# Kernel optimization log

Measured on AMD Instinct MI355X. Metric: run time of the kernel, lower is better.

The kernel has to match this reference:

```python
import jax, jax.numpy as jnp
import numpy as np

N_NODES = 100000
N_EDGES = 1600000
D_IN = 128
D_HID = 128
N_CLASSES = 10


def setup_inputs() -> dict:
    key = jax.random.key(0)
    ks = jax.random.split(key, 9)
    x = jax.random.normal(ks[0], (N_NODES, D_IN), dtype=jnp.float32)
    edge_index = jax.random.randint(ks[1], (2, N_EDGES), 0, N_NODES, dtype=jnp.int64)
    edge_attr = jax.random.uniform(ks[2], (N_EDGES,), dtype=jnp.float32)
    s1 = 1.0 / np.sqrt(D_IN)
    s2 = 1.0 / np.sqrt(D_HID)
    W1 = jax.random.uniform(ks[3], (D_IN, D_HID), jnp.float32, -s1, s1)
    b1 = jnp.zeros((D_HID,), jnp.float32)
    W2 = jax.random.uniform(ks[4], (D_HID, D_HID), jnp.float32, -s2, s2)
    b2 = jnp.zeros((D_HID,), jnp.float32)
    Wm = jax.random.uniform(ks[5], (D_HID, N_CLASSES), jnp.float32, -s2, s2)
    bm = jax.random.uniform(ks[6], (N_CLASSES,), jnp.float32, -s2, s2)
    return {"x": x, "edge_index": edge_index, "edge_attr": edge_attr,
            "W1": W1, "b1": b1, "W2": W2, "b2": b2, "Wm": Wm, "bm": bm}


def _gcn_norm(edge_index, edge_attr, n_nodes):
    # PyG GCNConv default: add self-loops (weight 1), symmetric normalization.
    src, dst = edge_index[0], edge_index[1]
    loop = jnp.arange(n_nodes, dtype=src.dtype)
    src_f = jnp.concatenate([src, loop])
    dst_f = jnp.concatenate([dst, loop])
    w = jnp.concatenate([edge_attr, jnp.ones((n_nodes,), edge_attr.dtype)])
    deg = jax.ops.segment_sum(w, dst_f, num_segments=n_nodes)  # in-degree
    dinv = jnp.where(deg > 0, jax.lax.rsqrt(deg), 0.0)
    norm = dinv[src_f] * w * dinv[dst_f]  # [E + N]
    return src_f, dst_f, norm


def _gcn_conv(x, src_f, dst_f, norm, W, b, n_nodes):
    h = x @ W                                   # [N, D] dense transform first
    msg = h[src_f] * norm[:, None]              # gather + scale  [E+N, D]
    agg = jax.ops.segment_sum(msg, dst_f, num_segments=n_nodes)  # scatter-add
    return agg + b


def reference(x, edge_index, edge_attr, W1, b1, W2, b2, Wm, bm):
    n = x.shape[0]
    src_f, dst_f, norm = _gcn_norm(edge_index, edge_attr, n)
    h = jax.nn.relu(_gcn_conv(x, src_f, dst_f, norm, W1, b1, n))
    h = jax.nn.relu(_gcn_conv(h, src_f, dst_f, norm, W2, b2, n))
    # F.dropout(training=False) is identity in eval mode
    pooled = jnp.mean(h, axis=0)                # global mean pool -> [D_HID]
    return pooled @ Wm + bm                     # [N_CLASSES]
```

## Files before the change

### kernel.cpp

```cpp
#include <hip/hip_runtime.h>

#define N_NODES_C 100000
#define N_EDGES_C 1600000
#define D_C 128
#define N_CLASSES_C 10
#define POOL_BLOCKS_C 1024
#define NBUCKET 391
#define BUCKET_CAP 4608
#define BPAD 16
#define EPB 4096
#define NB_A ((N_EDGES_C + EPB - 1) / EPB)

using bf16x8 = __attribute__((ext_vector_type(8))) short;
using f32x4  = __attribute__((ext_vector_type(4))) float;

__device__ __forceinline__ unsigned int pack_bf2(float a, float b) {
    unsigned int ua = __float_as_uint(a);
    unsigned int ub = __float_as_uint(b);
    ua = (ua + 0x7FFFu + ((ua >> 16) & 1u)) >> 16;
    ub = (ub + 0x7FFFu + ((ub >> 16) & 1u)) & 0xFFFF0000u;
    return ua | ub;
}

__device__ __forceinline__ void bf8_fma(uint4 r, float v, float* acc) {
    acc[0] = fmaf(v, __uint_as_float(r.x << 16), acc[0]);
    acc[1] = fmaf(v, __uint_as_float(r.x & 0xFFFF0000u), acc[1]);
    acc[2] = fmaf(v, __uint_as_float(r.y << 16), acc[2]);
    acc[3] = fmaf(v, __uint_as_float(r.y & 0xFFFF0000u), acc[3]);
    acc[4] = fmaf(v, __uint_as_float(r.z << 16), acc[4]);
    acc[5] = fmaf(v, __uint_as_float(r.z & 0xFFFF0000u), acc[5]);
    acc[6] = fmaf(v, __uint_as_float(r.w << 16), acc[6]);
    acc[7] = fmaf(v, __uint_as_float(r.w & 0xFFFF0000u), acc[7]);
}

__device__ __forceinline__ int edge_word(const int* __restrict__ ei, long long idx, int is64) {
    return is64 ? ei[2 * idx] : ei[idx];
}

__global__ void detect_init_kernel(const int* __restrict__ ei, int* __restrict__ flag,
                                   int* __restrict__ bcnt) {
    int t = threadIdx.x;
    if (blockIdx.x == 0) {
        if (t < 64) {
            int nz = 0;
            for (int i = t; i < 512; i += 64) nz |= ei[2 * i + 1];
            unsigned long long b = __ballot(nz != 0);
            if (t == 0) *flag = (b == 0ULL) ? 1 : 0;
        }
    } else {
        int i = (blockIdx.x - 1) * 256 + t;
        if (i < NBUCKET * BPAD) bcnt[i] = 0;
    }
}

__global__ __launch_bounds__(512) void bucket_fill_kernel(
        const int* __restrict__ ei, const float* __restrict__ attr,
        const int* __restrict__ flag, int* __restrict__ bcnt, int2* __restrict__ bkt) {
    __shared__ int2 stage[EPB];
    __shared__ unsigned short sbin[EPB];
    __shared__ int hist[512];
    __shared__ int lstart[512];
    __shared__ int cursor[NBUCKET];
    __shared__ int gbase[NBUCKET];

    const int t = threadIdx.x;
    const long long e0 = (long long)blockIdx.x * EPB;
    const int n = (N_EDGES_C - e0 < EPB) ? (int)(N_EDGES_C - e0) : EPB;
    const int is64 = *flag;

    hist[t] = 0;
    __syncthreads();

    int  myb[8];
    int2 myrec[8];
#pragma unroll
    for (int j = 0; j < 8; ++j) {
        int i = t + j * 512;
        myb[j] = -1;
        if (i < n) {
            long long e = e0 + i;
            int s = edge_word(ei, e, is64);
            int d = edge_word(ei, (long long)N_EDGES_C + e, is64);
            float a = attr[e];
            int b = d >> 8;
            myb[j] = b;
            myrec[j].x = s | ((d & 0xFF) << 17);
            myrec[j].y = __float_as_int(a);
            atomicAdd(&hist[b], 1);
        }
    }
    __syncthreads();

    const int myh = hist[t];
    lstart[t] = myh;
    __syncthreads();
    for (int off = 1; off < 512; off <<= 1) {
        int v = lstart[t];
        int add = (t >= off) ? lstart[t - off] : 0;
        __syncthreads();
        lstart[t] = v + add;
        __syncthreads();
    }
    int excl = lstart[t] - myh;
    if (t < NBUCKET) cursor[t] = excl;
    lstart[t] = excl;
    __syncthreads();

#pragma unroll
    for (int j = 0; j < 8; ++j) {
        if (myb[j] >= 0) {
            int slot = atomicAdd(&cursor[myb[j]], 1);
            stage[slot] = myrec[j];
            sbin[slot] = (unsigned short)myb[j];
        }
    }
    if (t < NBUCKET) {
        int k = myh;
        gbase[t] = k ? atomicAdd(&bcnt[t * BPAD], k) : 0;
    }
    __syncthreads();

    for (int i = t; i < n; i += 512) {
        int b = sbin[i];
        int local = gbase[b] + (i - lstart[b]);
        if (local < BUCKET_CAP)
            bkt[(long long)b * BUCKET_CAP + local] = stage[i];
    }
}

__global__ __launch_bounds__(256) void bucket_sort_kernel(
        const int* __restrict__ bcnt, int2* __restrict__ bkt,
        int2* __restrict__ rowinfo, float* __restrict__ dinv) {
    __shared__ int2 recA[BUCKET_CAP];
    __shared__ int2 recB[BUCKET_CAP];
    __shared__ int hist[256], lstart[256], cursor[256];
    __shared__ float degs[256];

    const int b = blockIdx.x, t = threadIdx.x;
    int n = bcnt[b * BPAD];
    if (n > BUCKET_CAP) n = BUCKET_CAP;
    int2* win = bkt + (long long)b * BUCKET_CAP;

    hist[t] = 0;
    degs[t] = 0.f;
    __syncthreads();

    for (int i = t; i < n; i += 256) {
        int2 cv = win[i];
        recA[i] = cv;
        int d = (cv.x >> 17) & 0xFF;
        atomicAdd(&hist[d], 1);
        atomicAdd(&degs[d], __int_as_float(cv.y));
    }
    __syncthreads();

    const int myh = hist[t];
    lstart[t] = myh;
    __syncthreads();
    for (int off = 1; off < 256; off <<= 1) {
        int v = lstart[t];
        int add = (t >= off) ? lstart[t - off] : 0;
        __syncthreads();
        lstart[t] = v + add;
        __syncthreads();
    }
    int excl = lstart[t] - myh;
    cursor[t] = excl;
    lstart[t] = excl;
    __syncthreads();

    for (int i = t; i < n; i += 256) {
        int2 cv = recA[i];
        int d = (cv.x >> 17) & 0xFF;
        int slot = atomicAdd(&cursor[d], 1);
        int2 o;
        o.x = cv.x & 0x1FFFF;
        o.y = cv.y;
        recB[slot] = o;
    }
    __syncthreads();

    for (int i = t; i < n; i += 256) win[i] = recB[i];

    int node = b * 256 + t;
    if (node < N_NODES_C) {
        int2 ri;
        ri.x = b * BUCKET_CAP + lstart[t];
        ri.y = myh;
        rowinfo[node] = ri;
        dinv[node] = rsqrtf(1.0f + degs[t]);
    }
}

__global__ __launch_bounds__(256) void convert_x_kernel(const float* __restrict__ x,
                                                        unsigned short* __restrict__ xb) {
    long long i = (long long)blockIdx.x * blockDim.x + threadIdx.x;
    const long long n8 = (long long)N_NODES_C * D_C / 8;
    if (i >= n8) return;
    const float4* p = (const float4*)x + i * 2;
    float4 a = p[0], b = p[1];
    uint4 o;
    o.x = pack_bf2(a.x, a.y);
    o.y = pack_bf2(a.z, a.w);
    o.z = pack_bf2(b.x, b.y);
    o.w = pack_bf2(b.z, b.w);
    ((uint4*)xb)[i] = o;
}

__global__ __launch_bounds__(256) void prep_w_kernel(const float* __restrict__ W1,
                                                     const float* __restrict__ W2,
                                                     unsigned short* __restrict__ Wp1,
                                                     unsigned short* __restrict__ Wp2) {
    const float* W = (blockIdx.x & 8) ? W2 : W1;
    unsigned short* Wp = (blockIdx.x & 8) ? Wp2 : Wp1;
    const int n = blockIdx.x & 7;
    const int t = threadIdx.x;
    const int s = t >> 6, l = t & 63;
    const int col = n * 16 + (l & 15);
    const int k0 = s * 32 + (l >> 4) * 8;
    float v[8];
#pragma unroll
    for (int j = 0; j < 8; ++j) v[j] = W[(k0 + j) * 128 + col];
    uint4 o;
    o.x = pack_bf2(v[0], v[1]);
    o.y = pack_bf2(v[2], v[3]);
    o.z = pack_bf2(v[4], v[5]);
    o.w = pack_bf2(v[6], v[7]);
    ((uint4*)Wp)[(n * 4 + s) * 64 + l] = o;
}

__global__ __launch_bounds__(256) void gemm_mfma(const unsigned short* __restrict__ A,
                                                 const unsigned short* __restrict__ Wp,
                                                 const float* __restrict__ dinv,
                                                 unsigned short* __restrict__ H,
                                                 int nrows) {
    __shared__ unsigned short Bl[2048 * 8];
    {
        const uint4* src = (const uint4*)Wp;
        uint4* dst = (uint4*)Bl;
        for (int i = threadIdx.x; i < 2048; i += 256) dst[i] = src[i];
    }
    __syncthreads();

    const int wid = threadIdx.x >> 6, lane = threadIdx.x & 63;
    const int rowA = lane & 15, kg = lane >> 4;
    const int r0 = blockIdx.x * 128 + wid * 32;

    bf16x8 afr[2][4];
#pragma unroll
    for (int m = 0; m < 2; ++m) {
        int row = r0 + m * 16 + rowA;
        if (row >= nrows) row = nrows - 1;
        const unsigned short* xp = A + (long long)row * D_C + kg * 8;
#pragma unroll
        for (int s = 0; s < 4; ++s) afr[m][s] = *(const bf16x8*)(xp + s * 32);
    }

    f32x4 acc[2][8];
#pragma unroll
    for (int m = 0; m < 2; ++m)
#pragma unroll
        for (int n = 0; n < 8; ++n) acc[m][n] = (f32x4){0.f, 0.f, 0.f, 0.f};

#pragma unroll
    for (int n = 0; n < 8; ++n) {
#pragma unroll
        for (int s = 0; s < 4; ++s) {
            bf16x8 bfr = *(const bf16x8*)(Bl + ((n * 4 + s) * 64 + lane) * 8);
            acc[0][n] = __builtin_amdgcn_mfma_f32_16x16x32_bf16(afr[0][s], bfr, acc[0][n], 0, 0, 0);
            acc[1][n] = __builtin_amdgcn_mfma_f32_16x16x32_bf16(afr[1][s], bfr, acc[1][n], 0, 0, 0);
        }
    }

    const int colb = lane & 15, rq = lane >> 4;
#pragma unroll
    for (int m = 0; m < 2; ++m) {
#pragma unroll
        for (int q = 0; q < 4; ++q) {
            int row = r0 + m * 16 + rq * 4 + q;
            if (row >= nrows) continue;
            float sc = dinv[row];
#pragma unroll
            for (int n = 0; n < 8; ++n) {
                unsigned int u = __float_as_uint(acc[m][n][q] * sc);
                u = (u + 0x7FFFu + ((u >> 16) & 1u)) >> 16;
                H[(long long)row * D_C + n * 16 + colb] = (unsigned short)u;
            }
        }
    }
}

template <int MODE>
__global__ __launch_bounds__(256) void agg_kernel(
        const unsigned short* __restrict__ h, const float* __restrict__ dinv,
        const int2* __restrict__ rowinfo, const int2* __restrict__ recs,
        const float* __restrict__ bias, void* __restrict__ out_v) {
    __shared__ float pool[128];
    if (MODE == 1) {
        if (threadIdx.x < 128) pool[threadIdx.x] = 0.f;
        __syncthreads();
    }
    const int g    = threadIdx.x >> 4;
    const int sub  = threadIdx.x & 15;
    const int lane = threadIdx.x & 63;
    const int grp  = lane >> 4;

    const float4 bA = *(const float4*)(bias + sub * 8);
    const float4 bB = *(const float4*)(bias + sub * 8 + 4);
    float p[8] = {0.f, 0.f, 0.f, 0.f, 0.f, 0.f, 0.f, 0.f};

    for (int i = blockIdx.x * 16 + g; i < N_NODES_C; i += gridDim.x * 16) {
        const float di = dinv[i];
        const int2 ri = rowinfo[i];
        const int2* row = recs + ri.x;
        const int m = ri.y;

        float acc[8] = {0.f, 0.f, 0.f, 0.f, 0.f, 0.f, 0.f, 0.f};
        {
            uint4 r = *(const uint4*)(h + (long long)i * D_C + sub * 8);
            bf8_fma(r, 1.0f, acc);
        }
        int j = 0;
        for (; j + 7 < m; j += 8) {
            int2 c0 = row[j + 0], c1 = row[j + 1], c2 = row[j + 2], c3 = row[j + 3];
            int2 c4 = row[j + 4], c5 = row[j + 5], c6 = row[j + 6], c7 = row[j + 7];
            uint4 r0 = *(const uint4*)(h + (long long)c0.x * D_C + sub * 8);
            uint4 r1 = *(const uint4*)(h + (long long)c1.x * D_C + sub * 8);
            uint4 r2 = *(const uint4*)(h + (long long)c2.x * D_C + sub * 8);
            uint4 r3 = *(const uint4*)(h + (long long)c3.x * D_C + sub * 8);
            uint4 r4 = *(const uint4*)(h + (long long)c4.x * D_C + sub * 8);
            uint4 r5 = *(const uint4*)(h + (long long)c5.x * D_C + sub * 8);
            uint4 r6 = *(const uint4*)(h + (long long)c6.x * D_C + sub * 8);
            uint4 r7 = *(const uint4*)(h + (long long)c7.x * D_C + sub * 8);
            bf8_fma(r0, __int_as_float(c0.y), acc);
            bf8_fma(r1, __int_as_float(c1.y), acc);
            bf8_fma(r2, __int_as_float(c2.y), acc);
            bf8_fma(r3, __int_as_float(c3.y), acc);
            bf8_fma(r4, __int_as_float(c4.y), acc);
            bf8_fma(r5, __int_as_float(c5.y), acc);
            bf8_fma(r6, __int_as_float(c6.y), acc);
            bf8_fma(r7, __int_as_float(c7.y), acc);
        }
        for (; j + 3 < m; j += 4) {
            int2 c0 = row[j + 0], c1 = row[j + 1], c2 = row[j + 2], c3 = row[j + 3];
            uint4 r0 = *(const uint4*)(h + (long long)c0.x * D_C + sub * 8);
            uint4 r1 = *(const uint4*)(h + (long long)c1.x * D_C + sub * 8);
            uint4 r2 = *(const uint4*)(h + (long long)c2.x * D_C + sub * 8);
            uint4 r3 = *(const uint4*)(h + (long long)c3.x * D_C + sub * 8);
            bf8_fma(r0, __int_as_float(c0.y), acc);
            bf8_fma(r1, __int_as_float(c1.y), acc);
            bf8_fma(r2, __int_as_float(c2.y), acc);
            bf8_fma(r3, __int_as_float(c3.y), acc);
        }
        for (; j < m; ++j) {
            int2 cv = row[j];
            uint4 r = *(const uint4*)(h + (long long)cv.x * D_C + sub * 8);
            bf8_fma(r, __int_as_float(cv.y), acc);
        }

        float o[8];
        o[0] = fmaxf(fmaf(acc[0], di, bA.x), 0.f);
        o[1] = fmaxf(fmaf(acc[1], di, bA.y), 0.f);
        o[2] = fmaxf(fmaf(acc[2], di, bA.z), 0.f);
        o[3] = fmaxf(fmaf(acc[3], di, bA.w), 0.f);
        o[4] = fmaxf(fmaf(acc[4], di, bB.x), 0.f);
        o[5] = fmaxf(fmaf(acc[5], di, bB.y), 0.f);
        o[6] = fmaxf(fmaf(acc[6], di, bB.z), 0.f);
        o[7] = fmaxf(fmaf(acc[7], di, bB.w), 0.f);

        if (MODE == 0) {
            uint4 pk;
            pk.x = pack_bf2(o[0], o[1]);
            pk.y = pack_bf2(o[2], o[3]);
            pk.z = pack_bf2(o[4], o[5]);
            pk.w = pack_bf2(o[6], o[7]);
            *(uint4*)((unsigned short*)out_v + (long long)i * D_C + sub * 8) = pk;
        } else {
#pragma unroll
            for (int k = 0; k < 8; ++k) p[k] += o[k];
        }
    }

    if (MODE == 1) {
#pragma unroll
        for (int k = 0; k < 8; ++k) {
            p[k] += __shfl_xor(p[k], 16);
            p[k] += __shfl_xor(p[k], 32);
        }
        if (grp == 0) {
#pragma unroll
            for (int k = 0; k < 8; ++k) atomicAdd(&pool[sub * 8 + k], p[k]);
        }
        __syncthreads();
        if (threadIdx.x < 128)
            ((float*)out_v)[blockIdx.x * 128 + threadIdx.x] = pool[threadIdx.x];
    }
}

__global__ __launch_bounds__(1024) void final_kernel(const float* __restrict__ part,
                                                     const float* __restrict__ Wm,
                                                     const float* __restrict__ bm,
                                                     float* __restrict__ out) {
    __shared__ float red[8][128];
    __shared__ float pooled[128];
    int t = threadIdx.x;
    int f = t & 127, c = t >> 7;
    float s = 0.f;
    for (int b = c; b < POOL_BLOCKS_C; b += 8) s += part[b * 128 + f];
    red[c][f] = s;
    __syncthreads();
    if (t < 128) {
        float tot = 0.f;
#pragma unroll
        for (int cc = 0; cc < 8; ++cc) tot += red[cc][t];
        pooled[t] = tot / (float)N_NODES_C;
    }
    __syncthreads();
    if (t < N_CLASSES_C) {
        float o = bm[t];
        for (int ff = 0; ff < 128; ++ff) o = fmaf(pooled[ff], Wm[ff * N_CLASSES_C + t], o);
        out[t] = o;
    }
}

extern "C" void kernel_launch(void* const* d_in, const int* in_sizes, int n_in,
                              void* d_out, int out_size, void* d_ws, size_t ws_size,
                              hipStream_t stream) {
    const float* x    = (const float*)d_in[0];
    const int*   ei   = (const int*)d_in[1];
    const float* attr = (const float*)d_in[2];
    const float* W1   = (const float*)d_in[3];
    const float* b1   = (const float*)d_in[4];
    const float* W2   = (const float*)d_in[5];
    const float* b2   = (const float*)d_in[6];
    const float* Wm   = (const float*)d_in[7];
    const float* bm   = (const float*)d_in[8];
    float* out = (float*)d_out;

    char* ws = (char*)d_ws;
    size_t off = 0;
    auto alloc = [&](size_t bytes) -> char* {
        char* p = ws + off;
        off += (bytes + 255) & ~(size_t)255;
        return p;
    };
    int*            flag    = (int*)alloc(4);
    int*            bcnt    = (int*)alloc((size_t)NBUCKET * BPAD * 4);
    int2*           rowinfo = (int2*)alloc((size_t)N_NODES_C * 8);
    float*          dinv    = (float*)alloc((size_t)N_NODES_C * 4);
    int2*           bkt     = (int2*)alloc((size_t)NBUCKET * BUCKET_CAP * 8);
    float*          part    = (float*)alloc((size_t)POOL_BLOCKS_C * 128 * 4);
    unsigned short* Wp1     = (unsigned short*)alloc(2048 * 8 * 2);
    unsigned short* Wp2     = (unsigned short*)alloc(2048 * 8 * 2);
    unsigned short* xb      = (unsigned short*)alloc((size_t)N_NODES_C * D_C * 2);
    unsigned short* hbuf    = (unsigned short*)alloc((size_t)N_NODES_C * D_C * 2);
    unsigned short* hb2     = (unsigned short*)alloc((size_t)N_NODES_C * D_C * 2);
    (void)ws_size;

    const int ntiles = (N_NODES_C + 127) / 128;
    const int agg_blocks = (N_NODES_C + 15) / 16;
    const int init_blocks = 1 + (NBUCKET * BPAD + 255) / 256;
    const int cvt_blocks = (int)(((long long)N_NODES_C * D_C / 8 + 255) / 256);

    detect_init_kernel<<<init_blocks, 256, 0, stream>>>(ei, flag, bcnt);
    bucket_fill_kernel<<<NB_A, 512, 0, stream>>>(ei, attr, flag, bcnt, bkt);
    bucket_sort_kernel<<<NBUCKET, 256, 0, stream>>>(bcnt, bkt, rowinfo, dinv);
    convert_x_kernel<<<cvt_blocks, 256, 0, stream>>>(x, xb);
    prep_w_kernel<<<16, 256, 0, stream>>>(W1, W2, Wp1, Wp2);

    gemm_mfma<<<ntiles, 256, 0, stream>>>(xb, Wp1, dinv, hbuf, N_NODES_C);
    agg_kernel<0><<<agg_blocks, 256, 0, stream>>>(hbuf, dinv, rowinfo, bkt, b1, hb2);
    gemm_mfma<<<ntiles, 256, 0, stream>>>(hb2, Wp2, dinv, hbuf, N_NODES_C);
    agg_kernel<1><<<POOL_BLOCKS_C, 256, 0, stream>>>(hbuf, dinv, rowinfo, bkt, b2, part);
    final_kernel<<<1, 1024, 0, stream>>>(part, Wm, bm, out);
}
```

Before: 247.9 us.

## Fuse x bf16 conversion into GEMM and process two nodes per group in aggregation

Drops the separate fp32-to-bf16 conversion kernel for x: the first GEMM now reads fp32 rows directly and packs them to bf16 in registers, which removes a full write and re-read of the converted array. The aggregation kernel has each 16-lane group handle two nodes at once, interleaving their edge gathers so more independent loads are in flight. The pooling grid is doubled to match. In exchange, the first GEMM reads twice as many A bytes, and the paired loop raises register pressure while degree imbalance between the two nodes leaves tail work unbalanced.

New measurement: 318.3 us. 28.4% more time.

```diff
diff --git a/kernel.cpp b/kernel.cpp
--- a/kernel.cpp
+++ b/kernel.cpp
@@ -4,7 +4,7 @@
 #define N_EDGES_C 1600000
 #define D_C 128
 #define N_CLASSES_C 10
-#define POOL_BLOCKS_C 1024
+#define POOL_BLOCKS_C 2048
 #define NBUCKET 391
 #define BUCKET_CAP 4608
 #define BPAD 16
@@ -192,21 +192,6 @@
     }
 }
 
-__global__ __launch_bounds__(256) void convert_x_kernel(const float* __restrict__ x,
-                                                        unsigned short* __restrict__ xb) {
-    long long i = (long long)blockIdx.x * blockDim.x + threadIdx.x;
-    const long long n8 = (long long)N_NODES_C * D_C / 8;
-    if (i >= n8) return;
-    const float4* p = (const float4*)x + i * 2;
-    float4 a = p[0], b = p[1];
-    uint4 o;
-    o.x = pack_bf2(a.x, a.y);
-    o.y = pack_bf2(a.z, a.w);
-    o.z = pack_bf2(b.x, b.y);
-    o.w = pack_bf2(b.z, b.w);
-    ((uint4*)xb)[i] = o;
-}
-
 __global__ __launch_bounds__(256) void prep_w_kernel(const float* __restrict__ W1,
                                                      const float* __restrict__ W2,
                                                      unsigned short* __restrict__ Wp1,
@@ -229,7 +214,8 @@
     ((uint4*)Wp)[(n * 4 + s) * 64 + l] = o;
 }
 
-__global__ __launch_bounds__(256) void gemm_mfma(const unsigned short* __restrict__ A,
+template <bool AF32>
+__global__ __launch_bounds__(256) void gemm_mfma(const void* __restrict__ A,
                                                  const unsigned short* __restrict__ Wp,
                                                  const float* __restrict__ dinv,
                                                  unsigned short* __restrict__ H,
@@ -251,9 +237,24 @@
     for (int m = 0; m < 2; ++m) {
         int row = r0 + m * 16 + rowA;
         if (row >= nrows) row = nrows - 1;
-        const unsigned short* xp = A + (long long)row * D_C + kg * 8;
-#pragma unroll
-        for (int s = 0; s < 4; ++s) afr[m][s] = *(const bf16x8*)(xp + s * 32);
+        if constexpr (AF32) {
+            const float* xp = (const float*)A + (long long)row * D_C + kg * 8;
+#pragma unroll
+            for (int s = 0; s < 4; ++s) {
+                float4 lo = *(const float4*)(xp + s * 32);
+                float4 hi = *(const float4*)(xp + s * 32 + 4);
+                uint4 pk;
+                pk.x = pack_bf2(lo.x, lo.y);
+                pk.y = pack_bf2(lo.z, lo.w);
+                pk.z = pack_bf2(hi.x, hi.y);
+                pk.w = pack_bf2(hi.z, hi.w);
+                afr[m][s] = __builtin_bit_cast(bf16x8, pk);
+            }
+        } else {
+            const unsigned short* xp = (const unsigned short*)A + (long long)row * D_C + kg * 8;
+#pragma unroll
+            for (int s = 0; s < 4; ++s) afr[m][s] = *(const bf16x8*)(xp + s * 32);
+        }
     }
 
     f32x4 acc[2][8];
@@ -288,6 +289,59 @@
             }
         }
     }
+}
+
+__device__ __forceinline__ void agg_edges(const unsigned short* __restrict__ h,
+                                          const int2* __restrict__ row,
+                                          int j, int m, int sub, float* acc) {
+    for (; j + 7 < m; j += 8) {
+        int2 c0 = row[j + 0], c1 = row[j + 1], c2 = row[j + 2], c3 = row[j + 3];
+        int2 c4 = row[j + 4], c5 = row[j + 5], c6 = row[j + 6], c7 = row[j + 7];
+        uint4 r0 = *(const uint4*)(h + (long long)c0.x * D_C + sub * 8);
+        uint4 r1 = *(const uint4*)(h + (long long)c1.x * D_C + sub * 8);
+        uint4 r2 = *(const uint4*)(h + (long long)c2.x * D_C + sub * 8);
+        uint4 r3 = *(const uint4*)(h + (long long)c3.x * D_C + sub * 8);
+        uint4 r4 = *(const uint4*)(h + (long long)c4.x * D_C + sub * 8);
+        uint4 r5 = *(const uint4*)(h + (long long)c5.x * D_C + sub * 8);
+        uint4 r6 = *(const uint4*)(h + (long long)c6.x * D_C + sub * 8);
+        uint4 r7 = *(const uint4*)(h + (long long)c7.x * D_C + sub * 8);
+        bf8_fma(r0, __int_as_float(c0.y), acc);
+        bf8_fma(r1, __int_as_float(c1.y), acc);
+        bf8_fma(r2, __int_as_float(c2.y), acc);
+        bf8_fma(r3, __int_as_float(c3.y), acc);
+        bf8_fma(r4, __int_as_float(c4.y), acc);
+        bf8_fma(r5, __int_as_float(c5.y), acc);
+        bf8_fma(r6, __int_as_float(c6.y), acc);
+        bf8_fma(r7, __int_as_float(c7.y), acc);
+    }
+    for (; j + 3 < m; j += 4) {
+        int2 c0 = row[j + 0], c1 = row[j + 1], c2 = row[j + 2], c3 = row[j + 3];
+        uint4 r0 = *(const uint4*)(h + (long long)c0.x * D_C + sub * 8);
+        uint4 r1 = *(const uint4*)(h + (long long)c1.x * D_C + sub * 8);
+        uint4 r2 = *(const uint4*)(h + (long long)c2.x * D_C + sub * 8);
+        uint4 r3 = *(const uint4*)(h + (long long)c3.x * D_C + sub * 8);
+        bf8_fma(r0, __int_as_float(c0.y), acc);
+        bf8_fma(r1, __int_as_float(c1.y), acc);
+        bf8_fma(r2, __int_as_float(c2.y), acc);
+        bf8_fma(r3, __int_as_float(c3.y), acc);
+    }
+    for (; j < m; ++j) {
+        int2 cv = row[j];
+        uint4 r = *(const uint4*)(h + (long long)cv.x * D_C + sub * 8);
+        bf8_fma(r, __int_as_float(cv.y), acc);
+    }
+}
+
+__device__ __forceinline__ void finish_node(const float* acc, float di,
+                                            float4 bA, float4 bB, float* o) {
+    o[0] = fmaxf(fmaf(acc[0], di, bA.x), 0.f);
+    o[1] = fmaxf(fmaf(acc[1], di, bA.y), 0.f);
+    o[2] = fmaxf(fmaf(acc[2], di, bA.z), 0.f);
+    o[3] = fmaxf(fmaf(acc[3], di, bA.w), 0.f);
+    o[4] = fmaxf(fmaf(acc[4], di, bB.x), 0.f);
+    o[5] = fmaxf(fmaf(acc[5], di, bB.y), 0.f);
+    o[6] = fmaxf(fmaf(acc[6], di, bB.z), 0.f);
+    o[7] = fmaxf(fmaf(acc[7], di, bB.w), 0.f);
 }
 
 template <int MODE>
@@ -305,79 +359,103 @@
     const int lane = threadIdx.x & 63;
     const int grp  = lane >> 4;
 
-    const float4 bA = *(const float4*)(bias + sub * 8);
-    const float4 bB = *(const float4*)(bias + sub * 8 + 4);
+    const float4 bA4 = *(const float4*)(bias + sub * 8);
+    const float4 bB4 = *(const float4*)(bias + sub * 8 + 4);
     float p[8] = {0.f, 0.f, 0.f, 0.f, 0.f, 0.f, 0.f, 0.f};
 
-    for (int i = blockIdx.x * 16 + g; i < N_NODES_C; i += gridDim.x * 16) {
-        const float di = dinv[i];
-        const int2 ri = rowinfo[i];
-        const int2* row = recs + ri.x;
-        const int m = ri.y;
-
-        float acc[8] = {0.f, 0.f, 0.f, 0.f, 0.f, 0.f, 0.f, 0.f};
+    for (int i0 = blockIdx.x * 32 + g * 2; i0 < N_NODES_C; i0 += gridDim.x * 32) {
+        const int iA = i0, iB = i0 + 1;
+        const bool hB = (iB < N_NODES_C);
+        const float diA = dinv[iA];
+        const int2 riA = rowinfo[iA];
+        float diB = 0.f;
+        int2 riB = riA;
+        if (hB) { diB = dinv[iB]; riB = rowinfo[iB]; }
+        const int2* rowA = recs + riA.x;
+        const int2* rowB = recs + riB.x;
+        const int mA = riA.y;
+        const int mB = hB ? riB.y : 0;
+
+        float accA[8] = {0.f, 0.f, 0.f, 0.f, 0.f, 0.f, 0.f, 0.f};
+        float accB[8] = {0.f, 0.f, 0.f, 0.f, 0.f, 0.f, 0.f, 0.f};
         {
-            uint4 r = *(const uint4*)(h + (long long)i * D_C + sub * 8);
-            bf8_fma(r, 1.0f, acc);
-        }
+            uint4 sA = *(const uint4*)(h + (long long)iA * D_C + sub * 8);
+            bf8_fma(sA, 1.0f, accA);
+            if (hB) {
+                uint4 sB = *(const uint4*)(h + (long long)iB * D_C + sub * 8);
+                bf8_fma(sB, 1.0f, accB);
+            }
+        }
+
         int j = 0;
-        for (; j + 7 < m; j += 8) {
-            int2 c0 = row[j + 0], c1 = row[j + 1], c2 = row[j + 2], c3 = row[j + 3];
-            int2 c4 = row[j + 4], c5 = row[j + 5], c6 = row[j + 6], c7 = row[j + 7];
-            uint4 r0 = *(const uint4*)(h + (long long)c0.x * D_C + sub * 8);
-            uint4 r1 = *(const uint4*)(h + (long long)c1.x * D_C + sub * 8);
-            uint4 r2 = *(const uint4*)(h + (long long)c2.x * D_C + sub * 8);
-            uint4 r3 = *(const uint4*)(h + (long long)c3.x * D_C + sub * 8);
-            uint4 r4 = *(const uint4*)(h + (long long)c4.x * D_C + sub * 8);
-            uint4 r5 = *(const uint4*)(h + (long long)c5.x * D_C + sub * 8);
-            uint4 r6 = *(const uint4*)(h + (long long)c6.x * D_C + sub * 8);
-            uint4 r7 = *(const uint4*)(h + (long long)c7.x * D_C + sub * 8);
-            bf8_fma(r0, __int_as_float(c0.y), acc);
-            bf8_fma(r1, __int_as_float(c1.y), acc);
-            bf8_fma(r2, __int_as_float(c2.y), acc);
-            bf8_fma(r3, __int_as_float(c3.y), acc);
-            bf8_fma(r4, __int_as_float(c4.y), acc);
-            bf8_fma(r5, __int_as_float(c5.y), acc);
-            bf8_fma(r6, __int_as_float(c6.y), acc);
-            bf8_fma(r7, __int_as_float(c7.y), acc);
-        }
-        for (; j + 3 < m; j += 4) {
-            int2 c0 = row[j + 0], c1 = row[j + 1], c2 = row[j + 2], c3 = row[j + 3];
-            uint4 r0 = *(const uint4*)(h + (long long)c0.x * D_C + sub * 8);
-            uint4 r1 = *(const uint4*)(h + (long long)c1.x * D_C + sub * 8);
-            uint4 r2 = *(const uint4*)(h + (long long)c2.x * D_C + sub * 8);
-            uint4 r3 = *(const uint4*)(h + (long long)c3.x * D_C + sub * 8);
-            bf8_fma(r0, __int_as_float(c0.y), acc);
-            bf8_fma(r1, __int_as_float(c1.y), acc);
-            bf8_fma(r2, __int_as_float(c2.y), acc);
-            bf8_fma(r3, __int_as_float(c3.y), acc);
-        }
-        for (; j < m; ++j) {
-            int2 cv = row[j];
-            uint4 r = *(const uint4*)(h + (long long)cv.x * D_C + sub * 8);
-            bf8_fma(r, __int_as_float(cv.y), acc);
-        }
-
-        float o[8];
-        o[0] = fmaxf(fmaf(acc[0], di, bA.x), 0.f);
-        o[1] = fmaxf(fmaf(acc[1], di, bA.y), 0.f);
-        o[2] = fmaxf(fmaf(acc[2], di, bA.z), 0.f);
-        o[3] = fmaxf(fmaf(acc[3], di, bA.w), 0.f);
-        o[4] = fmaxf(fmaf(acc[4], di, bB.x), 0.f);
-        o[5] = fmaxf(fmaf(acc[5], di, bB.y), 0.f);
-        o[6] = fmaxf(fmaf(acc[6], di, bB.z), 0.f);
-        o[7] = fmaxf(fmaf(acc[7], di, bB.w), 0.f);
+        const int mMin = (mA < mB) ? mA : mB;
+        for (; j + 7 < mMin; j += 8) {
+            int2 a0 = rowA[j + 0], a1 = rowA[j + 1], a2 = rowA[j + 2], a3 = rowA[j + 3];
+            int2 a4 = rowA[j + 4], a5 = rowA[j + 5], a6 = rowA[j + 6], a7 = rowA[j + 7];
+            int2 b0 = rowB[j + 0], b1 = rowB[j + 1], b2 = rowB[j + 2], b3 = rowB[j + 3];
+            int2 b4 = rowB[j + 4], b5 = rowB[j + 5], b6 = rowB[j + 6], b7 = rowB[j + 7];
+            uint4 ra0 = *(const uint4*)(h + (long long)a0.x * D_C + sub * 8);
+            uint4 ra1 = *(const uint4*)(h + (long long)a1.x * D_C + sub * 8);
+            uint4 ra2 = *(const uint4*)(h + (long long)a2.x * D_C + sub * 8);
+            uint4 ra3 = *(const uint4*)(h + (long long)a3.x * D_C + sub * 8);
+            uint4 ra4 = *(const uint4*)(h + (long long)a4.x * D_C + sub * 8);
+            uint4 ra5 = *(const uint4*)(h + (long long)a5.x * D_C + sub * 8);
+            uint4 ra6 = *(const uint4*)(h + (long long)a6.x * D_C + sub * 8);
+            uint4 ra7 = *(const uint4*)(h + (long long)a7.x * D_C + sub * 8);
+            uint4 rb0 = *(const uint4*)(h + (long long)b0.x * D_C + sub * 8);
+            uint4 rb1 = *(const uint4*)(h + (long long)b1.x * D_C + sub * 8);
+            uint4 rb2 = *(const uint4*)(h + (long long)b2.x * D_C + sub * 8);
+            uint4 rb3 = *(const uint4*)(h + (long long)b3.x * D_C + sub * 8);
+            uint4 rb4 = *(const uint4*)(h + (long long)b4.x * D_C + sub * 8);
+            uint4 rb5 = *(const uint4*)(h + (long long)b5.x * D_C + sub * 8);
+            uint4 rb6 = *(const uint4*)(h + (long long)b6.x * D_C + sub * 8);
+            uint4 rb7 = *(const uint4*)(h + (long long)b7.x * D_C + sub * 8);
+            bf8_fma(ra0, __int_as_float(a0.y), accA);
+            bf8_fma(ra1, __int_as_float(a1.y), accA);
+            bf8_fma(ra2, __int_as_float(a2.y), accA);
+            bf8_fma(ra3, __int_as_float(a3.y), accA);
+            bf8_fma(ra4, __int_as_float(a4.y), accA);
+            bf8_fma(ra5, __int_as_float(a5.y), accA);
+            bf8_fma(ra6, __int_as_float(a6.y), accA);
+            bf8_fma(ra7, __int_as_float(a7.y), accA);
+            bf8_fma(rb0, __int_as_float(b0.y), accB);
+            bf8_fma(rb1, __int_as_float(b1.y), accB);
+            bf8_fma(rb2, __int_as_float(b2.y), accB);
+            bf8_fma(rb3, __int_as_float(b3.y), accB);
+            bf8_fma(rb4, __int_as_float(b4.y), accB);
+            bf8_fma(rb5, __int_as_float(b5.y), accB);
+            bf8_fma(rb6, __int_as_float(b6.y), accB);
+            bf8_fma(rb7, __int_as_float(b7.y), accB);
+        }
+        agg_edges(h, rowA, j, mA, sub, accA);
+        if (hB) agg_edges(h, rowB, j, mB, sub, accB);
+
+        float oA[8], oB[8];
+        finish_node(accA, diA, bA4, bB4, oA);
+        if (hB) finish_node(accB, diB, bA4, bB4, oB);
 
         if (MODE == 0) {
             uint4 pk;
-            pk.x = pack_bf2(o[0], o[1]);
-            pk.y = pack_bf2(o[2], o[3]);
-            pk.z = pack_bf2(o[4], o[5]);
-            pk.w = pack_bf2(o[6], o[7]);
-            *(uint4*)((unsigned short*)out_v + (long long)i * D_C + sub * 8) = pk;
+            pk.x = pack_bf2(oA[0], oA[1]);
+            pk.y = pack_bf2(oA[2], oA[3]);
+            pk.z = pack_bf2(oA[4], oA[5]);
+            pk.w = pack_bf2(oA[6], oA[7]);
+            *(uint4*)((unsigned short*)out_v + (long long)iA * D_C + sub * 8) = pk;
+            if (hB) {
+                uint4 pk2;
+                pk2.x = pack_bf2(oB[0], oB[1]);
+                pk2.y = pack_bf2(oB[2], oB[3]);
+                pk2.z = pack_bf2(oB[4], oB[5]);
+                pk2.w = pack_bf2(oB[6], oB[7]);
+                *(uint4*)((unsigned short*)out_v + (long long)iB * D_C + sub * 8) = pk2;
+            }
         } else {
 #pragma unroll
-            for (int k = 0; k < 8; ++k) p[k] += o[k];
+            for (int k = 0; k < 8; ++k) p[k] += oA[k];
+            if (hB) {
+#pragma unroll
+                for (int k = 0; k < 8; ++k) p[k] += oB[k];
+            }
         }
     }
 
@@ -452,25 +530,22 @@
     float*          part    = (float*)alloc((size_t)POOL_BLOCKS_C * 128 * 4);
     unsigned short* Wp1     = (unsigned short*)alloc(2048 * 8 * 2);
     unsigned short* Wp2     = (unsigned short*)alloc(2048 * 8 * 2);
-    unsigned short* xb      = (unsigned short*)alloc((size_t)N_NODES_C * D_C * 2);
     unsigned short* hbuf    = (unsigned short*)alloc((size_t)N_NODES_C * D_C * 2);
     unsigned short* hb2     = (unsigned short*)alloc((size_t)N_NODES_C * D_C * 2);
     (void)ws_size;
 
     const int ntiles = (N_NODES_C + 127) / 128;
-    const int agg_blocks = (N_NODES_C + 15) / 16;
+    const int agg_blocks = (N_NODES_C + 31) / 32;
     const int init_blocks = 1 + (NBUCKET * BPAD + 255) / 256;
-    const int cvt_blocks = (int)(((long long)N_NODES_C * D_C / 8 + 255) / 256);
 
     detect_init_kernel<<<init_blocks, 256, 0, stream>>>(ei, flag, bcnt);
     bucket_fill_kernel<<<NB_A, 512, 0, stream>>>(ei, attr, flag, bcnt, bkt);
     bucket_sort_kernel<<<NBUCKET, 256, 0, stream>>>(bcnt, bkt, rowinfo, dinv);
-    convert_x_kernel<<<cvt_blocks, 256, 0, stream>>>(x, xb);
     prep_w_kernel<<<16, 256, 0, stream>>>(W1, W2, Wp1, Wp2);
 
-    gemm_mfma<<<ntiles, 256, 0, stream>>>(xb, Wp1, dinv, hbuf, N_NODES_C);
+    gemm_mfma<true><<<ntiles, 256, 0, stream>>>(x, Wp1, dinv, hbuf, N_NODES_C);
     agg_kernel<0><<<agg_blocks, 256, 0, stream>>>(hbuf, dinv, rowinfo, bkt, b1, hb2);
-    gemm_mfma<<<ntiles, 256, 0, stream>>>(hb2, Wp2, dinv, hbuf, N_NODES_C);
+    gemm_mfma<false><<<ntiles, 256, 0, stream>>>(hb2, Wp2, dinv, hbuf, N_NODES_C);
     agg_kernel<1><<<POOL_BLOCKS_C, 256, 0, stream>>>(hbuf, dinv, rowinfo, bkt, b2, part);
     final_kernel<<<1, 1024, 0, stream>>>(part, Wm, bm, out);
 }
```
